# Optimization experiments

Measured on AMD Instinct MI355X. Metric: run time of the kernel, lower is better.

The kernel has to match this reference:

```python
import jax, jax.numpy as jnp
import numpy as np


def setup_inputs() -> dict:
    key = jax.random.key(0)
    k1, k2 = jax.random.split(key)
    n, d, num_classes = 262144, 128, 512
    inputs = jax.random.normal(k1, (n, d), dtype=jnp.float32)
    targets = jax.random.randint(k2, (n,), 0, num_classes)
    return {"inputs": inputs, "targets": targets, "num_classes": num_classes}


def reference(inputs, targets, num_classes):
    beta = 0.1
    eps = 1e-12  # torch F.normalize default eps (norm clamped to min eps)
    # L2-normalize features
    x = inputs / jnp.maximum(jnp.linalg.norm(inputs, axis=1, keepdims=True), eps)  # [n, d]

    # Per-class centers: mean of normalized features, then L2-normalize, detached.
    ones = jnp.ones((x.shape[0],), dtype=x.dtype)
    counts = jax.ops.segment_sum(ones, targets, num_segments=num_classes)          # [C]
    csum = jax.ops.segment_sum(x, targets, num_segments=num_classes)               # [C, d]
    cmean = csum / jnp.maximum(counts, 1.0)[:, None]
    centers = cmean / jnp.maximum(jnp.linalg.norm(cmean, axis=1, keepdims=True), eps)
    centers = jax.lax.stop_gradient(centers)  # .detach() in original

    # Numerator logit: center of own class dotted with own feature
    pos = jnp.sum(centers[targets] * x, axis=1) / beta                             # [n]
    # Denominator: sum of exp over all *present* classes (original only builds
    # centers for pids that appear in the batch)
    scores = jnp.exp(centers @ x.T / beta)                                         # [C, n]
    present = counts > 0
    denom = jnp.sum(jnp.where(present[:, None], scores, 0.0), axis=0)              # [n]
    return -jnp.mean(pos - jnp.log(denom))
```

## Files before the change

kernel.cpp:

```cpp
#include <hip/hip_runtime.h>
#include <stdint.h>

#define NROWS 262144
#define DDIM 128
#define NCLS 512
#define NHB 64
constexpr float INV_BETA = 10.0f;
constexpr float EXP2_SCALE = 14.426950408889634f;

typedef __bf16 v8bf __attribute__((ext_vector_type(8)));
typedef float v4f __attribute__((ext_vector_type(4)));

__device__ inline unsigned short f2bf(float f) {
    uint32_t u = __builtin_bit_cast(uint32_t, f);
    u += 0x7FFFu + ((u >> 16) & 1u);
    return (unsigned short)(u >> 16);
}
__device__ inline float bflo(uint32_t u) { return __builtin_bit_cast(float, u << 16); }
__device__ inline float bfhi(uint32_t u) { return __builtin_bit_cast(float, u & 0xFFFF0000u); }

#define GLL16(gsrc, ldst)                                                        \
    __builtin_amdgcn_global_load_lds(                                            \
        (const __attribute__((address_space(1))) void*)(uintptr_t)(gsrc),        \
        (__attribute__((address_space(3))) void*)(uintptr_t)(ldst), 16, 0, 0)

__global__ __launch_bounds__(256) void k1_normalize(
    const float* __restrict__ in, const int* __restrict__ tgt,
    unsigned short* __restrict__ xb, int* __restrict__ bh) {
    __shared__ int h[NCLS];
    int t = threadIdx.x;
    if (blockIdx.x >= 8192) {
        int b = blockIdx.x - 8192;
        for (int i = t; i < NCLS; i += 256) h[i] = 0;
        __syncthreads();
        int base = b * (NROWS / NHB);
        for (int i = base + t; i < base + NROWS / NHB; i += 256)
            atomicAdd(&h[tgt[i]], 1);
        __syncthreads();
        for (int i = t; i < NCLS; i += 256)
            bh[b * NCLS + i] = h[i];
        return;
    }
    int w = t >> 6;
    int half = (t & 63) >> 5;
    int lane32 = t & 31;
    int hw = blockIdx.x * 8 + w * 2 + half;
    int r0 = hw * 4;
    float4 v[4];
#pragma unroll
    for (int j = 0; j < 4; ++j)
        v[j] = *reinterpret_cast<const float4*>(in + (size_t)(r0 + j) * DDIM + lane32 * 4);
    float s[4];
#pragma unroll
    for (int j = 0; j < 4; ++j)
        s[j] = v[j].x * v[j].x + v[j].y * v[j].y + v[j].z * v[j].z + v[j].w * v[j].w;
#pragma unroll
    for (int off = 1; off < 32; off <<= 1) {
#pragma unroll
        for (int j = 0; j < 4; ++j) s[j] += __shfl_xor(s[j], off);
    }
#pragma unroll
    for (int j = 0; j < 4; ++j) {
        float iv = rsqrtf(fmaxf(s[j], 1e-24f));
        ushort4 o;
        o.x = f2bf(v[j].x * iv); o.y = f2bf(v[j].y * iv);
        o.z = f2bf(v[j].z * iv); o.w = f2bf(v[j].w * iv);
        *reinterpret_cast<ushort4*>(xb + (size_t)(r0 + j) * DDIM + lane32 * 4) = o;
    }
}

__global__ __launch_bounds__(512) void k_prefix(
    const int* __restrict__ bh, int* __restrict__ counts, int* __restrict__ offs,
    int* __restrict__ base, float* __restrict__ nabsG, float* __restrict__ out) {
    __shared__ int sc[NCLS];
    __shared__ int za;
    int t = threadIdx.x;
    int cnt = 0;
#pragma unroll 8
    for (int b = 0; b < NHB; ++b) cnt += bh[b * NCLS + t];
    counts[t] = cnt;
    sc[t] = cnt;
    if (t == 0) za = 0;
    __syncthreads();
    for (int off = 1; off < NCLS; off <<= 1) {
        int v = (t >= off) ? sc[t - off] : 0;
        __syncthreads();
        sc[t] += v;
        __syncthreads();
    }
    int excl = sc[t] - cnt;
    offs[t] = excl;
    if (cnt == 0) atomicAdd(&za, 1);
    int run = excl;
    for (int b = 0; b < NHB; ++b) {
        base[b * NCLS + t] = run;
        run += bh[b * NCLS + t];
    }
    __syncthreads();
    if (t == 0) { *nabsG = (float)za; *out = 0.0f; }
}

__global__ __launch_bounds__(256) void k_scatter(
    const int* __restrict__ tgt, const int* __restrict__ base, int* __restrict__ ridx) {
    __shared__ int cur[NCLS];
    int t = threadIdx.x;
    int b = blockIdx.x;
    cur[t] = base[b * NCLS + t];
    cur[t + 256] = base[b * NCLS + t + 256];
    __syncthreads();
    int r0 = b * (NROWS / NHB);
    for (int i = t; i < NROWS / NHB; i += 256) {
        int row = r0 + i;
        int c = tgt[row];
        int pos = atomicAdd(&cur[c], 1);
        ridx[pos] = row;
    }
}

__global__ __launch_bounds__(512) void k_centers(
    const unsigned short* __restrict__ xb, const int* __restrict__ ridx,
    const int* __restrict__ counts, const int* __restrict__ offs,
    unsigned short* __restrict__ cen, float* __restrict__ out) {
    __shared__ float2 sP[8][64];
    int t = threadIdx.x, w = t >> 6, l = t & 63;
    int cl = blockIdx.x;
    int cnt = counts[cl], start = offs[cl];
    const uint32_t* xb32 = (const uint32_t*)xb;
    float a0 = 0.0f, a1 = 0.0f;
    int per = (cnt + 7) >> 3;
    int lo = w * per, hi = min(cnt, lo + per);
    int i = lo;
    for (; i + 8 <= hi; i += 8) {
        int id[8]; uint32_t v[8];
#pragma unroll
        for (int j = 0; j < 8; ++j) id[j] = ridx[start + i + j];
#pragma unroll
        for (int j = 0; j < 8; ++j) v[j] = xb32[(size_t)id[j] * 64 + l];
#pragma unroll
        for (int j = 0; j < 8; ++j) { a0 += bflo(v[j]); a1 += bfhi(v[j]); }
    }
    for (; i < hi; ++i) {
        uint32_t v = xb32[(size_t)ridx[start + i] * 64 + l];
        a0 += bflo(v); a1 += bfhi(v);
    }
    sP[w][l] = make_float2(a0, a1);
    __syncthreads();
    if (w == 0) {
        float c0 = 0.0f, c1 = 0.0f;
#pragma unroll
        for (int q = 0; q < 8; ++q) { c0 += sP[q][l].x; c1 += sP[q][l].y; }
        float fc = fmaxf((float)cnt, 1.0f);
        c0 /= fc; c1 /= fc;
        float ss = c0 * c0 + c1 * c1;
        for (int off = 1; off < 64; off <<= 1) ss += __shfl_xor(ss, off);
        float inv = 1.0f / fmaxf(sqrtf(ss), 1e-12f);
        ushort2 o;
        o.x = f2bf(c0 * inv); o.y = f2bf(c1 * inv);
        *reinterpret_cast<ushort2*>(cen + (size_t)cl * DDIM + l * 2) = o;
        if (l == 0)
            atomicAdd(out, -(float)cnt * sqrtf(ss) * (INV_BETA / (float)NROWS));
    }
}

__global__ __launch_bounds__(1024) void k4_loss(
    const unsigned short* __restrict__ xb, const unsigned short* __restrict__ cen,
    const float* __restrict__ nabsG, float* __restrict__ out) {
    extern __shared__ char lds[];
    char* xL0 = lds;
    char* xL1 = lds + 32768;
    float* denP = (float*)(lds + 65536);
    float* wsum = (float*)(lds + 73728);
    int t = threadIdx.x, w = t >> 6, l = t & 63;
    int lm = l & 15, lk = l >> 4;
    float nabs = *nabsG;

    v8bf afr[2][4];
#pragma unroll
    for (int m = 0; m < 2; ++m)
#pragma unroll
        for (int kc = 0; kc < 4; ++kc) {
            int arow = w * 32 + m * 16 + lm;
            afr[m][kc] = *reinterpret_cast<const v8bf*>(cen + (size_t)arow * DDIM + kc * 32 + lk * 8);
        }

    int block0 = blockIdx.x * 1024;
    const char* xbB = (const char*)xb + (size_t)block0 * 256;

    int C0 = w * 128 + l;
    int C1 = C0 + 64;
    int so0 = (C0 >> 4) * 256 + ((((C0 & 15) ^ ((C0 >> 4) & 7))) << 4);
    int so1 = (C1 >> 4) * 256 + ((((C1 & 15) ^ ((C1 >> 4) & 7))) << 4);
    int dw = w * 2048;

    GLL16(xbB + so0, xL0 + dw);
    GLL16(xbB + so1, xL0 + dw + 1024);
    float lossAcc = 0.0f;
    asm volatile("s_waitcnt vmcnt(0)" ::: "memory");
    __syncthreads();

    for (int tile = 0; tile < 8; ++tile) {
        char* xc = (tile & 1) ? xL1 : xL0;
        char* xn = (tile & 1) ? xL0 : xL1;
        if (tile < 7) {
            const char* s = xbB + (size_t)(tile + 1) * 32768;
            GLL16(s + so0, xn + dw);
            GLL16(s + so1, xn + dw + 1024);
        }

#pragma unroll
        for (int h = 0; h < 2; ++h) {
            v4f acc[2][4];
            v4f zero = {0.0f, 0.0f, 0.0f, 0.0f};
#pragma unroll
            for (int m = 0; m < 2; ++m)
#pragma unroll
                for (int n = 0; n < 4; ++n) acc[m][n] = zero;

#pragma unroll
            for (int kc = 0; kc < 4; ++kc) {
                int kb = kc * 64 + lk * 16;
                v8bf b[4];
#pragma unroll
                for (int n = 0; n < 4; ++n) {
                    int brow = h * 64 + n * 16 + lm;
                    b[n] = *reinterpret_cast<const v8bf*>(xc + brow * 256 + (kb ^ ((brow & 7) << 4)));
                }
#pragma unroll
                for (int m = 0; m < 2; ++m)
#pragma unroll
                    for (int n = 0; n < 4; ++n)
                        acc[m][n] = __builtin_amdgcn_mfma_f32_16x16x32_bf16(afr[m][kc], b[n], acc[m][n], 0, 0, 0);
            }

#pragma unroll
            for (int n = 0; n < 4; ++n) {
                float se = 0.0f;
#pragma unroll
                for (int m = 0; m < 2; ++m) {
#pragma unroll
                    for (int rr = 0; rr < 4; ++rr)
                        se += __builtin_amdgcn_exp2f(acc[m][n][rr] * EXP2_SCALE);
                }
                se += __shfl_xor(se, 16); se += __shfl_xor(se, 32);
                if (l < 16) denP[w * 128 + h * 64 + n * 16 + lm] = se;
            }
        }
        asm volatile("s_waitcnt vmcnt(0)" ::: "memory");
        __syncthreads();
        if (t < 128) {
            float den = 0.0f;
#pragma unroll
            for (int q = 0; q < 16; ++q) den += denP[q * 128 + t];
            lossAcc += __logf(den - nabs);
        }
        __syncthreads();
    }
    if (t < 128) {
#pragma unroll
        for (int off = 1; off < 64; off <<= 1) lossAcc += __shfl_xor(lossAcc, off);
        if (l == 0) wsum[w] = lossAcc;
    }
    __syncthreads();
    if (t == 0) atomicAdd(out, (wsum[0] + wsum[1]) * (1.0f / NROWS));
}

extern "C" void kernel_launch(void* const* d_in, const int* in_sizes, int n_in,
                              void* d_out, int out_size, void* d_ws, size_t ws_size,
                              hipStream_t stream) {
    const float* in = (const float*)d_in[0];
    const int* tgt = (const int*)d_in[1];
    float* out = (float*)d_out;
    char* ws = (char*)d_ws;
    unsigned short* xb = (unsigned short*)(ws);
    int* counts = (int*)(ws + 67108864);
    int* offs = (int*)(ws + 67110912);
    float* nabsG = (float*)(ws + 67112960);
    unsigned short* cen = (unsigned short*)(ws + 67115264);
    int* ridx = (int*)(ws + 67246336);
    int* bh = (int*)(ws + 68294912);
    int* base = (int*)(ws + 68557056);

    (void)hipFuncSetAttribute((const void*)k4_loss,
                              hipFuncAttributeMaxDynamicSharedMemorySize, 73792);

    hipLaunchKernelGGL(k1_normalize, dim3(8192 + NHB), dim3(256), 0, stream, in, tgt, xb, bh);
    hipLaunchKernelGGL(k_prefix, dim3(1), dim3(512), 0, stream, bh, counts, offs, base, nabsG, out);
    hipLaunchKernelGGL(k_scatter, dim3(NHB), dim3(256), 0, stream, tgt, base, ridx);
    hipLaunchKernelGGL(k_centers, dim3(NCLS), dim3(512), 0, stream, xb, ridx, counts, offs, cen, out);
    hipLaunchKernelGGL(k4_loss, dim3(256), dim3(1024), 73792, stream, xb, cen, nabsG, out);
}
```

Before: 112.8 us.

## Fold exp2 scale into centers and double-buffer denominator partials to drop a barrier

The centers kernel now writes centers pre-multiplied by the base-2 exponent scale, so the loss kernel no longer multiplies each score before exp2. The denominator partial buffer is double-buffered by tile parity. This lets all 16 warps reduce row denominators with shuffles, instead of only two waves, and removes the second barrier per tile. The cost is more LDS, a wider final reduction across 16 warp sums, and storing scaled centers in bf16.

After: 111.4 us. About the same (-1.2%).

```diff
diff --git a/kernel.cpp b/kernel.cpp
--- a/kernel.cpp
+++ b/kernel.cpp
@@ -153,7 +153,7 @@
         c0 /= fc; c1 /= fc;
         float ss = c0 * c0 + c1 * c1;
         for (int off = 1; off < 64; off <<= 1) ss += __shfl_xor(ss, off);
-        float inv = 1.0f / fmaxf(sqrtf(ss), 1e-12f);
+        float inv = EXP2_SCALE / fmaxf(sqrtf(ss), 1e-12f);
         ushort2 o;
         o.x = f2bf(c0 * inv); o.y = f2bf(c1 * inv);
         *reinterpret_cast<ushort2*>(cen + (size_t)cl * DDIM + l * 2) = o;
@@ -169,7 +169,7 @@
     char* xL0 = lds;
     char* xL1 = lds + 32768;
     float* denP = (float*)(lds + 65536);
-    float* wsum = (float*)(lds + 73728);
+    float* wsum = (float*)(lds + 81920);
     int t = threadIdx.x, w = t >> 6, l = t & 63;
     int lm = l & 15, lk = l >> 4;
     float nabs = *nabsG;
@@ -195,12 +195,15 @@
     GLL16(xbB + so0, xL0 + dw);
     GLL16(xbB + so1, xL0 + dw + 1024);
     float lossAcc = 0.0f;
+    int rs = w * 8 + (l >> 3);
+    int rq = (l & 7) * 2;
     asm volatile("s_waitcnt vmcnt(0)" ::: "memory");
     __syncthreads();
 
     for (int tile = 0; tile < 8; ++tile) {
         char* xc = (tile & 1) ? xL1 : xL0;
         char* xn = (tile & 1) ? xL0 : xL1;
+        float* dp = denP + (tile & 1) * 2048;
         if (tile < 7) {
             const char* s = xbB + (size_t)(tile + 1) * 32768;
             GLL16(s + so0, xn + dw);
@@ -239,29 +242,31 @@
                 for (int m = 0; m < 2; ++m) {
 #pragma unroll
                     for (int rr = 0; rr < 4; ++rr)
-                        se += __builtin_amdgcn_exp2f(acc[m][n][rr] * EXP2_SCALE);
+                        se += __builtin_amdgcn_exp2f(acc[m][n][rr]);
                 }
                 se += __shfl_xor(se, 16); se += __shfl_xor(se, 32);
-                if (l < 16) denP[w * 128 + h * 64 + n * 16 + lm] = se;
+                if (l < 16) dp[w * 128 + h * 64 + n * 16 + lm] = se;
             }
         }
         asm volatile("s_waitcnt vmcnt(0)" ::: "memory");
         __syncthreads();
-        if (t < 128) {
-            float den = 0.0f;
-#pragma unroll
-            for (int q = 0; q < 16; ++q) den += denP[q * 128 + t];
-            lossAcc += __logf(den - nabs);
-        }
-        __syncthreads();
-    }
-    if (t < 128) {
-#pragma unroll
-        for (int off = 1; off < 64; off <<= 1) lossAcc += __shfl_xor(lossAcc, off);
-        if (l == 0) wsum[w] = lossAcc;
-    }
-    __syncthreads();
-    if (t == 0) atomicAdd(out, (wsum[0] + wsum[1]) * (1.0f / NROWS));
+        float den = dp[rq * 128 + rs] + dp[(rq + 1) * 128 + rs];
+        den += __shfl_xor(den, 1);
+        den += __shfl_xor(den, 2);
+        den += __shfl_xor(den, 4);
+        if ((l & 7) == 0) lossAcc += __logf(den - nabs);
+    }
+    lossAcc += __shfl_xor(lossAcc, 8);
+    lossAcc += __shfl_xor(lossAcc, 16);
+    lossAcc += __shfl_xor(lossAcc, 32);
+    if (l == 0) wsum[w] = lossAcc;
+    __syncthreads();
+    if (t == 0) {
+        float s = 0.0f;
+#pragma unroll
+        for (int q = 0; q < 16; ++q) s += wsum[q];
+        atomicAdd(out, s * (1.0f / NROWS));
+    }
 }
 
 extern "C" void kernel_launch(void* const* d_in, const int* in_sizes, int n_in,
@@ -281,11 +286,11 @@
     int* base = (int*)(ws + 68557056);
 
     (void)hipFuncSetAttribute((const void*)k4_loss,
-                              hipFuncAttributeMaxDynamicSharedMemorySize, 73792);
+                              hipFuncAttributeMaxDynamicSharedMemorySize, 81984);
 
     hipLaunchKernelGGL(k1_normalize, dim3(8192 + NHB), dim3(256), 0, stream, in, tgt, xb, bh);
     hipLaunchKernelGGL(k_prefix, dim3(1), dim3(512), 0, stream, bh, counts, offs, base, nabsG, out);
     hipLaunchKernelGGL(k_scatter, dim3(NHB), dim3(256), 0, stream, tgt, base, ridx);
     hipLaunchKernelGGL(k_centers, dim3(NCLS), dim3(512), 0, stream, xb, ridx, counts, offs, cen, out);
-    hipLaunchKernelGGL(k4_loss, dim3(256), dim3(1024), 73792, stream, xb, cen, nabsG, out);
-}
+    hipLaunchKernelGGL(k4_loss, dim3(256), dim3(1024), 81984, stream, xb, cen, nabsG, out);
+}
```
